# Performance work log

Measured on AMD Instinct MI355X. Metric: run time of the kernel, lower is better.

The kernel has to match this reference:

```python
import jax, jax.numpy as jnp
import numpy as np

EMB = 1024
HEADS = 16
HEAD_DIM = EMB // HEADS
MASK_VAL = -10000.0


def setup_inputs() -> dict:
    key = jax.random.key(0)
    ks = jax.random.split(key, 5)
    B, S = 4, 2048
    x = jax.random.normal(ks[0], (B, S, EMB), dtype=jnp.float32)
    scale = 1.0 / np.sqrt(EMB)
    w_qkv = jax.random.normal(ks[1], (EMB, 3 * EMB), dtype=jnp.float32) * scale
    b_qkv = jnp.zeros((3 * EMB,), dtype=jnp.float32)
    w_fc = jax.random.normal(ks[2], (EMB, EMB), dtype=jnp.float32) * scale
    b_fc = jnp.zeros((EMB,), dtype=jnp.float32)
    return {"x": x, "w_qkv": w_qkv, "b_qkv": b_qkv, "w_fc": w_fc, "b_fc": b_fc}


def reference(x, w_qkv, b_qkv, w_fc, b_fc):
    B, S, _ = x.shape
    qkv = x @ w_qkv + b_qkv                      # (B, S, 3*EMB)
    q, k, v = jnp.split(qkv, 3, axis=-1)
    # split heads: (B, S, EMB) -> (B, H, S, Dh)
    def sh(t):
        return t.reshape(B, S, HEADS, HEAD_DIM).transpose(0, 2, 1, 3)
    q, k, v = sh(q), sh(k), sh(v)
    scores = jnp.einsum('bhqd,bhkd->bhqk', q, k) / np.sqrt(HEAD_DIM)
    causal = jnp.tril(jnp.ones((S, S), dtype=bool))[None, None]
    scores = jnp.where(causal, scores, jnp.float32(MASK_VAL))
    probs = jax.nn.softmax(scores, axis=-1)
    out = jnp.einsum('bhqk,bhkd->bhqd', probs, v)
    out = out.transpose(0, 2, 1, 3).reshape(B, S, EMB)  # merge heads
    return out @ w_fc + b_fc
```

## Files before the change

kernel.cpp:

```cpp
#include <hip/hip_runtime.h>
#include <hip/hip_bf16.h>
#include <cstdint>

#define BF16 __hip_bfloat16

typedef __attribute__((ext_vector_type(8))) short bhalf8;
typedef __attribute__((ext_vector_type(4))) float floatx4;

#define MFMA16(a, b, c) __builtin_amdgcn_mfma_f32_16x16x32_bf16((a), (b), (c), 0, 0, 0)

#define MASKV (-30000.0f)
#define QSCALE 0.18033688011112042f

__device__ __forceinline__ bhalf8 cvt8(const float* p) {
  const float4 f0 = *(const float4*)p;
  const float4 f1 = *(const float4*)(p + 4);
  union { bhalf8 v; ushort u[8]; } r;
  const float t[8] = {f0.x, f0.y, f0.z, f0.w, f1.x, f1.y, f1.z, f1.w};
#pragma unroll
  for (int i = 0; i < 8; ++i) {
    BF16 h = __float2bfloat16(t[i]);
    r.u[i] = *(const ushort*)&h;
  }
  return r.v;
}

__global__ void cvt_f32_bf16(const float* __restrict__ in, BF16* __restrict__ out) {
  const size_t i = ((size_t)blockIdx.x * 256 + threadIdx.x) * 8;
  *(bhalf8*)(out + i) = cvt8(in + i);
}

__global__ void transpose_cvt(const float* __restrict__ in, ushort* __restrict__ out,
                              int R, int C) {
  __shared__ ushort t[32][33];
  const int c0 = blockIdx.x * 32, r0 = blockIdx.y * 32;
  const int tx = threadIdx.x, ty = threadIdx.y;
#pragma unroll
  for (int j = 0; j < 32; j += 8) {
    BF16 h = __float2bfloat16(in[(size_t)(r0 + ty + j) * C + c0 + tx]);
    t[ty + j][tx] = *(const ushort*)&h;
  }
  __syncthreads();
#pragma unroll
  for (int j = 0; j < 32; j += 8)
    out[(size_t)(c0 + ty + j) * R + r0 + tx] = t[tx][ty + j];
}

template <int MODE>
__global__ __launch_bounds__(256, 2) void gemm_bt(
    const BF16* __restrict__ A, const BF16* __restrict__ Bt, const float* __restrict__ bias,
    void* __restrict__ C0v, BF16* __restrict__ C1, BF16* __restrict__ C2,
    int Md, int Nd, int Kd) {
  __shared__ __align__(16) BF16 As[128 * 64];
  __shared__ __align__(16) BF16 Bs[128 * 64];

  const int tid = threadIdx.x;
  const int w = tid >> 6, lane = tid & 63;
  const int lm = lane & 15, quad = lane >> 4;
  const int wm = (w >> 1) * 64, wn = (w & 1) * 64;
  const int tile_m = blockIdx.y * 128, tile_n = blockIdx.x * 128;

  floatx4 acc[4][4];
#pragma unroll
  for (int i = 0; i < 4; ++i)
#pragma unroll
    for (int j = 0; j < 4; ++j) acc[i][j] = (floatx4){0.f, 0.f, 0.f, 0.f};

  int srow[4], sgs[4], sslot[4];
#pragma unroll
  for (int j = 0; j < 4; ++j) {
    const int slot = (j * 4 + w) * 64 + lane;
    sslot[j] = slot;
    srow[j] = slot >> 3;
    sgs[j] = ((slot & 7) - (slot >> 3)) & 7;
  }

  bhalf8 va[4], vb[4], nva[4], nvb[4];
#pragma unroll
  for (int j = 0; j < 4; ++j) {
    va[j] = *(const bhalf8*)(A + (size_t)(tile_m + srow[j]) * Kd + sgs[j] * 8);
    vb[j] = *(const bhalf8*)(Bt + (size_t)(tile_n + srow[j]) * Kd + sgs[j] * 8);
  }

  for (int k0 = 0; k0 < Kd; k0 += 64) {
    __syncthreads();
#pragma unroll
    for (int j = 0; j < 4; ++j) {
      *(bhalf8*)(As + sslot[j] * 8) = va[j];
      *(bhalf8*)(Bs + sslot[j] * 8) = vb[j];
    }
    __syncthreads();

    if (k0 + 64 < Kd) {
      const int k1 = k0 + 64;
#pragma unroll
      for (int j = 0; j < 4; ++j) {
        nva[j] = *(const bhalf8*)(A + (size_t)(tile_m + srow[j]) * Kd + k1 + sgs[j] * 8);
        nvb[j] = *(const bhalf8*)(Bt + (size_t)(tile_n + srow[j]) * Kd + k1 + sgs[j] * 8);
      }
    }

#pragma unroll
    for (int s = 0; s < 2; ++s) {
      bhalf8 af[4], bfr[4];
#pragma unroll
      for (int mt = 0; mt < 4; ++mt) {
        const int r = wm + mt * 16 + lm;
        const int g = ((s * 4 + quad) + r) & 7;
        af[mt] = *(const bhalf8*)(As + r * 64 + g * 8);
      }
#pragma unroll
      for (int nt = 0; nt < 4; ++nt) {
        const int r = wn + nt * 16 + lm;
        const int g = ((s * 4 + quad) + r) & 7;
        bfr[nt] = *(const bhalf8*)(Bs + r * 64 + g * 8);
      }
#pragma unroll
      for (int mt = 0; mt < 4; ++mt)
#pragma unroll
        for (int nt = 0; nt < 4; ++nt)
          acc[mt][nt] = MFMA16(af[mt], bfr[nt], acc[mt][nt]);
    }
#pragma unroll
    for (int j = 0; j < 4; ++j) { va[j] = nva[j]; vb[j] = nvb[j]; }
  }

#pragma unroll
  for (int nt = 0; nt < 4; ++nt) {
    const int n = tile_n + wn + nt * 16 + lm;
    const float bv = bias[n];
#pragma unroll
    for (int mt = 0; mt < 4; ++mt) {
      const int m0 = tile_m + wm + mt * 16 + quad * 4;
      floatx4 v = acc[mt][nt];
      if (MODE == 0) {
        float* C0f = (float*)C0v;
#pragma unroll
        for (int r = 0; r < 4; ++r)
          C0f[(size_t)(m0 + r) * Nd + n] = v[r] + bv;
      } else {
        const int which = n >> 10;
        const int h = (n >> 6) & 15;
        const int d = n & 63;
        if (which == 2) {
          const int b = m0 >> 11, s0 = m0 & 2047;
          union { ushort4 u4; ushort u[4]; } pk;
#pragma unroll
          for (int r = 0; r < 4; ++r) {
            BF16 hv = __float2bfloat16(v[r] + bv);
            pk.u[r] = *(const ushort*)&hv;
          }
          *(ushort4*)(C2 + ((size_t)((b * 16 + h) * 64 + d)) * 2048 + s0) = pk.u4;
        } else {
          BF16* dst = (which == 0) ? (BF16*)C0v : C1;
          const float sc = (which == 0) ? QSCALE : 1.0f;
#pragma unroll
          for (int r = 0; r < 4; ++r) {
            const int m = m0 + r, b = m >> 11, si = m & 2047;
            dst[((size_t)(b * 16 + h) * 2048 + si) * 64 + d] =
                __float2bfloat16((v[r] + bv) * sc);
          }
        }
      }
    }
  }
}

__global__ __launch_bounds__(256, 2) void flash_attn(
    const BF16* __restrict__ Q, const BF16* __restrict__ Kmat,
    const BF16* __restrict__ VT, BF16* __restrict__ O) {
  __shared__ __align__(16) BF16 Ps[4][4][16 * 64];

  const int tid = threadIdx.x;
  const int w = tid >> 6, lane = tid & 63;
  const int lm = lane & 15, quad = lane >> 4;
  const int bh = blockIdx.y;
  const int x = blockIdx.x;
  const int qt = (w == 0) ? x : (w == 1) ? (15 - x) : (w == 2) ? (16 + x) : (31 - x);
  const int qb0 = qt * 64;
  const size_t bh_off = (size_t)bh * (2048 * 64);

  bhalf8 aq[4][2];
#pragma unroll
  for (int s2 = 0; s2 < 4; ++s2) {
    const BF16* qp = Q + bh_off + (size_t)(qb0 + s2 * 16 + lm) * 64 + quad * 8;
    aq[s2][0] = *(const bhalf8*)qp;
    aq[s2][1] = *(const bhalf8*)(qp + 32);
  }

  floatx4 oacc[4][4];
  float m_i[4], l_i[4];
#pragma unroll
  for (int s2 = 0; s2 < 4; ++s2) {
    m_i[s2] = MASKV;
    l_i[s2] = 0.f;
#pragma unroll
    for (int i = 0; i < 4; ++i) oacc[s2][i] = (floatx4){0.f, 0.f, 0.f, 0.f};
  }

  for (int kt = 0; kt <= qt; ++kt) {
    const int k0 = kt * 64;

    bhalf8 ak[4][2], av[4][2];
#pragma unroll
    for (int nt = 0; nt < 4; ++nt) {
      const BF16* kp = Kmat + bh_off + (size_t)(k0 + nt * 16 + lm) * 64 + quad * 8;
      ak[nt][0] = *(const bhalf8*)kp;
      ak[nt][1] = *(const bhalf8*)(kp + 32);
      const BF16* vp = VT + bh_off + (size_t)(nt * 16 + lm) * 2048 + k0 + quad * 8;
      av[nt][0] = *(const bhalf8*)vp;
      av[nt][1] = *(const bhalf8*)(vp + 32);
    }

#pragma unroll
    for (int s2 = 0; s2 < 4; ++s2) {
      const int qb = qb0 + s2 * 16;
      if (k0 > qb + 15) continue;

      floatx4 st[4];
#pragma unroll
      for (int nt = 0; nt < 4; ++nt) {
        floatx4 z = (floatx4){0.f, 0.f, 0.f, 0.f};
        z = MFMA16(ak[nt][0], aq[s2][0], z);
        z = MFMA16(ak[nt][1], aq[s2][1], z);
        st[nt] = z;
      }

      if (k0 + 63 > qb) {
#pragma unroll
        for (int nt = 0; nt < 4; ++nt)
#pragma unroll
          for (int r = 0; r < 4; ++r)
            if ((k0 + nt * 16 + quad * 4 + r) > (qb + lm)) st[nt][r] = MASKV;
      }

      float mx = MASKV;
#pragma unroll
      for (int nt = 0; nt < 4; ++nt)
#pragma unroll
        for (int r = 0; r < 4; ++r) mx = fmaxf(mx, st[nt][r]);
      mx = fmaxf(mx, __shfl_xor(mx, 16, 64));
      mx = fmaxf(mx, __shfl_xor(mx, 32, 64));
      const float mnew = fmaxf(m_i[s2], mx);
      const float alpha = __builtin_amdgcn_exp2f(m_i[s2] - mnew);
      m_i[s2] = mnew;

      float rs = 0.f;
#pragma unroll
      for (int nt = 0; nt < 4; ++nt)
#pragma unroll
        for (int r = 0; r < 4; ++r) {
          const float p = __builtin_amdgcn_exp2f(st[nt][r] - mnew);
          st[nt][r] = p;
          rs += p;
        }
      rs += __shfl_xor(rs, 16, 64);
      rs += __shfl_xor(rs, 32, 64);
      l_i[s2] = l_i[s2] * alpha + rs;
#pragma unroll
      for (int dn = 0; dn < 4; ++dn) oacc[s2][dn] *= alpha;

      BF16* pws = Ps[w][s2];
#pragma unroll
      for (int nt = 0; nt < 4; ++nt) {
        union { ushort4 u4; ushort u[4]; } pk;
#pragma unroll
        for (int r = 0; r < 4; ++r) {
          BF16 h = __float2bfloat16(st[nt][r]);
          pk.u[r] = *(const ushort*)&h;
        }
        const int g = ((nt * 2 + (quad >> 1)) + lm) & 7;
        *(ushort4*)(pws + lm * 64 + g * 8 + (quad & 1) * 4) = pk.u4;
      }

      const bhalf8 ap0 = *(const bhalf8*)(pws + lm * 64 + ((quad + lm) & 7) * 8);
      const bhalf8 ap1 = *(const bhalf8*)(pws + lm * 64 + ((4 + quad + lm) & 7) * 8);
#pragma unroll
      for (int dn = 0; dn < 4; ++dn) {
        oacc[s2][dn] = MFMA16(av[dn][0], ap0, oacc[s2][dn]);
        oacc[s2][dn] = MFMA16(av[dn][1], ap1, oacc[s2][dn]);
      }
    }
  }

  const int b = bh >> 4, h = bh & 15;
#pragma unroll
  for (int s2 = 0; s2 < 4; ++s2) {
    const float inv_l = 1.0f / l_i[s2];
    const size_t orow = (size_t)(b * 2048 + qb0 + s2 * 16 + lm) * 1024 + h * 64;
#pragma unroll
    for (int dn = 0; dn < 4; ++dn) {
      union { ushort4 u4; ushort u[4]; } pk;
#pragma unroll
      for (int r = 0; r < 4; ++r) {
        BF16 h2 = __float2bfloat16(oacc[s2][dn][r] * inv_l);
        pk.u[r] = *(const ushort*)&h2;
      }
      *(ushort4*)(O + orow + dn * 16 + quad * 4) = pk.u4;
    }
  }
}

extern "C" void kernel_launch(void* const* d_in, const int* in_sizes, int n_in,
                              void* d_out, int out_size, void* d_ws, size_t ws_size,
                              hipStream_t stream) {
  const float* x = (const float*)d_in[0];
  const float* w_qkv = (const float*)d_in[1];
  const float* b_qkv = (const float*)d_in[2];
  const float* w_fc = (const float*)d_in[3];
  const float* b_fc = (const float*)d_in[4];
  float* out = (float*)d_out;

  BF16* ws = (BF16*)d_ws;
  BF16* wTqkv = ws;
  BF16* wTfc = wTqkv + 3072 * 1024;
  BF16* xb = wTfc + 1024 * 1024;
  BF16* Qb = xb + 8388608;
  BF16* Kb = Qb + 8388608;
  BF16* VTb = Kb + 8388608;
  BF16* Ob = VTb + 8388608;

  cvt_f32_bf16<<<4096, 256, 0, stream>>>(x, xb);
  transpose_cvt<<<dim3(96, 32), dim3(32, 8), 0, stream>>>(w_qkv, (ushort*)wTqkv, 1024, 3072);
  transpose_cvt<<<dim3(32, 32), dim3(32, 8), 0, stream>>>(w_fc, (ushort*)wTfc, 1024, 1024);

  gemm_bt<1><<<dim3(24, 64), 256, 0, stream>>>(
      xb, wTqkv, b_qkv, (void*)Qb, Kb, VTb, 8192, 3072, 1024);
  flash_attn<<<dim3(8, 64), 256, 0, stream>>>(Qb, Kb, VTb, Ob);
  gemm_bt<0><<<dim3(8, 64), 256, 0, stream>>>(
      Ob, wTfc, b_fc, (void*)out, nullptr, nullptr, 8192, 1024, 1024);
}
```

Measured before the change: 280.2 us.

## Widen flash-attention KV tile to 128 and remap blocks per XCD

The flash attention kernel now processes 128 keys per iteration instead of 64, halving the number of online-softmax rescale and reduction steps per query row. Causal skipping moves to 16-key granularity. The V loads are split out and issued after the P tiles are written to LDS, which doubles the LDS P buffer. The grid is flattened to 1D, and each block is remapped so all blocks of one batch-head land on the same XCD for L2 locality of K/V. The trade-off is higher register pressure (8 K fragments plus 16 V fragments) and a larger LDS footprint, which may affect occupancy.

Result: slower. 492.6 us (+75.8%).

```diff
diff --git a/kernel.cpp b/kernel.cpp
--- a/kernel.cpp
+++ b/kernel.cpp
@@ -169,15 +169,21 @@
 __global__ __launch_bounds__(256, 2) void flash_attn(
     const BF16* __restrict__ Q, const BF16* __restrict__ Kmat,
     const BF16* __restrict__ VT, BF16* __restrict__ O) {
-  __shared__ __align__(16) BF16 Ps[4][4][16 * 64];
+  __shared__ __align__(16) BF16 Ps[4][4][16 * 128];
 
   const int tid = threadIdx.x;
   const int w = tid >> 6, lane = tid & 63;
   const int lm = lane & 15, quad = lane >> 4;
-  const int bh = blockIdx.y;
-  const int x = blockIdx.x;
+
+  const int bid = blockIdx.x;
+  const int xcd = bid & 7;
+  const int li = bid >> 3;
+  const int bh = xcd * 8 + (li >> 3);
+  const int x = li & 7;
+
   const int qt = (w == 0) ? x : (w == 1) ? (15 - x) : (w == 2) ? (16 + x) : (31 - x);
   const int qb0 = qt * 64;
+  const int ntiles = ((qb0 + 63) >> 7) + 1;
   const size_t bh_off = (size_t)bh * (2048 * 64);
 
   bhalf8 aq[4][2];
@@ -198,45 +204,44 @@
     for (int i = 0; i < 4; ++i) oacc[s2][i] = (floatx4){0.f, 0.f, 0.f, 0.f};
   }
 
-  for (int kt = 0; kt <= qt; ++kt) {
-    const int k0 = kt * 64;
-
-    bhalf8 ak[4][2], av[4][2];
-#pragma unroll
-    for (int nt = 0; nt < 4; ++nt) {
-      const BF16* kp = Kmat + bh_off + (size_t)(k0 + nt * 16 + lm) * 64 + quad * 8;
-      ak[nt][0] = *(const bhalf8*)kp;
-      ak[nt][1] = *(const bhalf8*)(kp + 32);
-      const BF16* vp = VT + bh_off + (size_t)(nt * 16 + lm) * 2048 + k0 + quad * 8;
-      av[nt][0] = *(const bhalf8*)vp;
-      av[nt][1] = *(const bhalf8*)(vp + 32);
+  for (int kt = 0; kt < ntiles; ++kt) {
+    const int k0 = kt * 128;
+
+    bhalf8 ak[8][2];
+#pragma unroll
+    for (int nt = 0; nt < 8; ++nt) {
+      if (k0 + nt * 16 <= qb0 + 63) {
+        const BF16* kp = Kmat + bh_off + (size_t)(k0 + nt * 16 + lm) * 64 + quad * 8;
+        ak[nt][0] = *(const bhalf8*)kp;
+        ak[nt][1] = *(const bhalf8*)(kp + 32);
+      }
     }
 
 #pragma unroll
     for (int s2 = 0; s2 < 4; ++s2) {
       const int qb = qb0 + s2 * 16;
-      if (k0 > qb + 15) continue;
-
-      floatx4 st[4];
-#pragma unroll
-      for (int nt = 0; nt < 4; ++nt) {
-        floatx4 z = (floatx4){0.f, 0.f, 0.f, 0.f};
-        z = MFMA16(ak[nt][0], aq[s2][0], z);
-        z = MFMA16(ak[nt][1], aq[s2][1], z);
-        st[nt] = z;
-      }
-
-      if (k0 + 63 > qb) {
-#pragma unroll
-        for (int nt = 0; nt < 4; ++nt)
-#pragma unroll
-          for (int r = 0; r < 4; ++r)
-            if ((k0 + nt * 16 + quad * 4 + r) > (qb + lm)) st[nt][r] = MASKV;
+
+      floatx4 st[8];
+#pragma unroll
+      for (int nt = 0; nt < 8; ++nt) {
+        if (k0 + nt * 16 <= qb + 15) {
+          floatx4 z = (floatx4){0.f, 0.f, 0.f, 0.f};
+          z = MFMA16(ak[nt][0], aq[s2][0], z);
+          z = MFMA16(ak[nt][1], aq[s2][1], z);
+          if (k0 + nt * 16 + 15 > qb) {
+#pragma unroll
+            for (int r = 0; r < 4; ++r)
+              if ((k0 + nt * 16 + quad * 4 + r) > (qb + lm)) z[r] = MASKV;
+          }
+          st[nt] = z;
+        } else {
+          st[nt] = (floatx4){MASKV, MASKV, MASKV, MASKV};
+        }
       }
 
       float mx = MASKV;
 #pragma unroll
-      for (int nt = 0; nt < 4; ++nt)
+      for (int nt = 0; nt < 8; ++nt)
 #pragma unroll
         for (int r = 0; r < 4; ++r) mx = fmaxf(mx, st[nt][r]);
       mx = fmaxf(mx, __shfl_xor(mx, 16, 64));
@@ -247,7 +252,7 @@
 
       float rs = 0.f;
 #pragma unroll
-      for (int nt = 0; nt < 4; ++nt)
+      for (int nt = 0; nt < 8; ++nt)
 #pragma unroll
         for (int r = 0; r < 4; ++r) {
           const float p = __builtin_amdgcn_exp2f(st[nt][r] - mnew);
@@ -262,24 +267,48 @@
 
       BF16* pws = Ps[w][s2];
 #pragma unroll
-      for (int nt = 0; nt < 4; ++nt) {
+      for (int nt = 0; nt < 8; ++nt) {
         union { ushort4 u4; ushort u[4]; } pk;
 #pragma unroll
         for (int r = 0; r < 4; ++r) {
           BF16 h = __float2bfloat16(st[nt][r]);
           pk.u[r] = *(const ushort*)&h;
         }
-        const int g = ((nt * 2 + (quad >> 1)) + lm) & 7;
-        *(ushort4*)(pws + lm * 64 + g * 8 + (quad & 1) * 4) = pk.u4;
-      }
-
-      const bhalf8 ap0 = *(const bhalf8*)(pws + lm * 64 + ((quad + lm) & 7) * 8);
-      const bhalf8 ap1 = *(const bhalf8*)(pws + lm * 64 + ((4 + quad + lm) & 7) * 8);
-#pragma unroll
-      for (int dn = 0; dn < 4; ++dn) {
-        oacc[s2][dn] = MFMA16(av[dn][0], ap0, oacc[s2][dn]);
-        oacc[s2][dn] = MFMA16(av[dn][1], ap1, oacc[s2][dn]);
-      }
+        const int g = ((nt * 2 + (quad >> 1)) + lm) & 15;
+        *(ushort4*)(pws + lm * 128 + g * 8 + (quad & 1) * 4) = pk.u4;
+      }
+    }
+
+    bhalf8 av[4][4];
+#pragma unroll
+    for (int j = 0; j < 4; ++j) {
+      if (k0 + j * 32 <= qb0 + 63) {
+#pragma unroll
+        for (int dn = 0; dn < 4; ++dn) {
+          const BF16* vp = VT + bh_off + (size_t)(dn * 16 + lm) * 2048 + k0 + j * 32 + quad * 8;
+          av[dn][j] = *(const bhalf8*)vp;
+        }
+      }
+    }
+
+#pragma unroll
+    for (int s2 = 0; s2 < 4; ++s2) {
+      const int qb = qb0 + s2 * 16;
+      const BF16* pws = Ps[w][s2];
+      bhalf8 ap[4];
+#pragma unroll
+      for (int j = 0; j < 4; ++j) {
+        if (k0 + j * 32 <= qb + 15) {
+          const int g = (j * 4 + quad + lm) & 15;
+          ap[j] = *(const bhalf8*)(pws + lm * 128 + g * 8);
+        }
+      }
+#pragma unroll
+      for (int dn = 0; dn < 4; ++dn)
+#pragma unroll
+        for (int j = 0; j < 4; ++j)
+          if (k0 + j * 32 <= qb + 15)
+            oacc[s2][dn] = MFMA16(av[dn][j], ap[j], oacc[s2][dn]);
     }
   }
 
@@ -326,7 +355,7 @@
 
   gemm_bt<1><<<dim3(24, 64), 256, 0, stream>>>(
       xb, wTqkv, b_qkv, (void*)Qb, Kb, VTb, 8192, 3072, 1024);
-  flash_attn<<<dim3(8, 64), 256, 0, stream>>>(Qb, Kb, VTb, Ob);
+  flash_attn<<<dim3(512), 256, 0, stream>>>(Qb, Kb, VTb, Ob);
   gemm_bt<0><<<dim3(8, 64), 256, 0, stream>>>(
       Ob, wTfc, b_fc, (void*)out, nullptr, nullptr, 8192, 1024, 1024);
 }
```
